# Optimization experiments

Measured on AMD Instinct MI355X. Metric: run time of the kernel, lower is better.

## Reference

```python
import jax, jax.numpy as jnp
import numpy as np

SIGMA_BOOST = 2.0   # sparse-hyper util.SIGMA_BOOST
EPSILON = 1e-6      # sparse-hyper util.EPSILON (10e-7)
B, N = 512, 16384   # batch, size


def setup_inputs() -> dict:
    key = jax.random.key(0)
    k1, k2, k3, k4, k5 = jax.random.split(key, 5)
    return {
        "x": jax.random.normal(k1, (B, N), jnp.float32),
        "noise": jax.random.normal(k2, (B, N, 2), jnp.float32),
        "pmeans": jax.random.normal(k3, (N, 2), jnp.float32),
        "psigmas": jax.random.normal(k4, (N,), jnp.float32),
        "pvalues": jax.random.normal(k5, (N,), jnp.float32),
    }


def reference(x, noise, pmeans, psigmas, pvalues):
    b, n = x.shape
    s = jnp.float32(n)  # square size (n, n); both dims equal
    # hyper(): transform_means = sigmoid * (size-1); transform_sigmas = (softplus(.+boost)+eps) * size
    means = jax.nn.sigmoid(pmeans)[None] * (s - 1.0)                    # (1, n, 2) -> bcast (b, n, 2)
    sigmas = (jax.nn.softplus(psigmas + SIGMA_BOOST) + EPSILON)[None, :, None] * s  # (1, n, 1)
    # Normal(means, sigmas).sample() -- non-differentiable sample
    samples = jax.lax.stop_gradient(means + sigmas * noise)             # (b, n, 2)
    # round, clamp to [0, n-1]
    indices = jnp.clip(jnp.round(samples).astype(jnp.int32), 0, n - 1)  # (b, n, 2)
    rows, cols = indices[..., 0], indices[..., 1]                       # (b, n) each
    values = jnp.broadcast_to(pvalues[None, :], (b, n))
    # sparse.contract: y[b, rows[b,t]] += values[b,t] * x[b, cols[b,t]]
    contrib = values * jnp.take_along_axis(x, cols, axis=1)             # (b, n)
    y = jnp.zeros((b, n), x.dtype).at[jnp.arange(b)[:, None], rows].add(contrib)
    return y
```

## Files before the change

kernel.cpp:

```cpp
#include <hip/hip_runtime.h>
#include <math.h>

#define SIGMA_BOOST 2.0f
#define EPSILON 1e-6f

__global__ void params_kernel(const float2* __restrict__ pmeans,
                              const float* __restrict__ psigmas,
                              const float* __restrict__ pvalues,
                              float4* __restrict__ params, int N) {
    int t = blockIdx.x * blockDim.x + threadIdx.x;
    if (t >= N) return;
    float2 pm = pmeans[t];
    float scale = (float)(N - 1);
    float m0 = __fmul_rn(__fdiv_rn(1.0f, __fadd_rn(1.0f, expf(-pm.x))), scale);
    float m1 = __fmul_rn(__fdiv_rn(1.0f, __fadd_rn(1.0f, expf(-pm.y))), scale);
    float z  = __fadd_rn(psigmas[t], SIGMA_BOOST);
    float sp = __fadd_rn(fmaxf(z, 0.0f), log1pf(expf(-fabsf(z))));
    float sg = __fmul_rn(__fadd_rn(sp, EPSILON), (float)N);
    params[t] = make_float4(m0, m1, sg, pvalues[t]);
}

template <bool INLINE_PARAMS>
__launch_bounds__(1024, 1)
__global__ void contract_kernel(const float* __restrict__ x,
                                const float2* __restrict__ noise,
                                const float4* __restrict__ params,
                                const float2* __restrict__ pmeans,
                                const float* __restrict__ psigmas,
                                const float* __restrict__ pvalues,
                                float* __restrict__ y, int N) {
    extern __shared__ float ly[];
    const int b = blockIdx.x;
    const int tid = threadIdx.x;
    const int nthr = blockDim.x;

    float4* ly4 = (float4*)ly;
    const int n4 = N >> 2;
    for (int i = tid; i < n4; i += nthr) ly4[i] = make_float4(0.f, 0.f, 0.f, 0.f);
    __syncthreads();

    const float*  xb = x + (size_t)b * N;
    const float2* nb = noise + (size_t)b * N;
    const float fN1 = (float)(N - 1);

    for (int t = tid; t < N; t += nthr) {
        float m0, m1, sg, pv;
        if (INLINE_PARAMS) {
            float2 pm = pmeans[t];
            float scale = (float)(N - 1);
            m0 = __fmul_rn(__fdiv_rn(1.0f, __fadd_rn(1.0f, expf(-pm.x))), scale);
            m1 = __fmul_rn(__fdiv_rn(1.0f, __fadd_rn(1.0f, expf(-pm.y))), scale);
            float z  = __fadd_rn(psigmas[t], SIGMA_BOOST);
            float sp = __fadd_rn(fmaxf(z, 0.0f), log1pf(expf(-fabsf(z))));
            sg = __fmul_rn(__fadd_rn(sp, EPSILON), (float)N);
            pv = pvalues[t];
        } else {
            float4 p = params[t];
            m0 = p.x; m1 = p.y; sg = p.z; pv = p.w;
        }
        float2 nz = nb[t];
        float s0 = __fadd_rn(m0, __fmul_rn(sg, nz.x));
        float s1 = __fadd_rn(m1, __fmul_rn(sg, nz.y));
        int row = (int)fminf(fmaxf(rintf(s0), 0.0f), fN1);
        int col = (int)fminf(fmaxf(rintf(s1), 0.0f), fN1);
        float contrib = __fmul_rn(pv, xb[col]);
        atomicAdd(&ly[row], contrib);
    }
    __syncthreads();

    float4* yb4 = (float4*)(y + (size_t)b * N);
    for (int i = tid; i < n4; i += nthr) yb4[i] = ly4[i];
}

extern "C" void kernel_launch(void* const* d_in, const int* in_sizes, int n_in,
                              void* d_out, int out_size, void* d_ws, size_t ws_size,
                              hipStream_t stream) {
    const float*  x       = (const float*)d_in[0];
    const float2* noise   = (const float2*)d_in[1];
    const float2* pmeans  = (const float2*)d_in[2];
    const float*  psigmas = (const float*)d_in[3];
    const float*  pvalues = (const float*)d_in[4];
    float* y = (float*)d_out;

    const int N = in_sizes[3];
    const int B = in_sizes[0] / N;

    const size_t params_bytes = (size_t)N * sizeof(float4);
    const bool use_ws = (ws_size >= params_bytes) && (d_ws != nullptr);

    const int block = 1024;
    const size_t lds_bytes = (size_t)N * sizeof(float);

    if (use_ws) {
        float4* params = (float4*)d_ws;
        params_kernel<<<(N + 255) / 256, 256, 0, stream>>>(pmeans, psigmas,
                                                           pvalues, params, N);
        contract_kernel<false><<<B, block, lds_bytes, stream>>>(
            x, noise, params, nullptr, nullptr, nullptr, y, N);
    } else {
        contract_kernel<true><<<B, block, lds_bytes, stream>>>(
            x, noise, nullptr, pmeans, psigmas, pvalues, y, N);
    }
}
```

Before: 163.4 us.

## Stage x row in LDS and unroll contract loop with vectorized noise loads

Copies each batch row of x into shared memory next to the accumulator, so the random column gathers hit LDS instead of global memory. The main loop is unrolled so each thread handles several consecutive elements, loading noise as float4 and grouping the gathers and atomics. Staging needs 128 KB of LDS per block and runs only when the device reports enough; otherwise a non-staged unroll-by-8 path runs. The extra LDS per block may lower occupancy, and each launch now makes host-side attribute queries.

```diff
diff --git a/kernel.cpp b/kernel.cpp
--- a/kernel.cpp
+++ b/kernel.cpp
@@ -4,12 +4,10 @@
 #define SIGMA_BOOST 2.0f
 #define EPSILON 1e-6f
 
-__global__ void params_kernel(const float2* __restrict__ pmeans,
-                              const float* __restrict__ psigmas,
-                              const float* __restrict__ pvalues,
-                              float4* __restrict__ params, int N) {
-    int t = blockIdx.x * blockDim.x + threadIdx.x;
-    if (t >= N) return;
+__device__ __forceinline__ float4 compute_param(const float2* __restrict__ pmeans,
+                                                const float* __restrict__ psigmas,
+                                                const float* __restrict__ pvalues,
+                                                int t, int N) {
     float2 pm = pmeans[t];
     float scale = (float)(N - 1);
     float m0 = __fmul_rn(__fdiv_rn(1.0f, __fadd_rn(1.0f, expf(-pm.x))), scale);
@@ -17,10 +15,18 @@
     float z  = __fadd_rn(psigmas[t], SIGMA_BOOST);
     float sp = __fadd_rn(fmaxf(z, 0.0f), log1pf(expf(-fabsf(z))));
     float sg = __fmul_rn(__fadd_rn(sp, EPSILON), (float)N);
-    params[t] = make_float4(m0, m1, sg, pvalues[t]);
+    return make_float4(m0, m1, sg, pvalues[t]);
 }
 
-template <bool INLINE_PARAMS>
+__global__ void params_kernel(const float2* __restrict__ pmeans,
+                              const float* __restrict__ psigmas,
+                              const float* __restrict__ pvalues,
+                              float4* __restrict__ params, int N) {
+    int t = blockIdx.x * blockDim.x + threadIdx.x;
+    if (t < N) params[t] = compute_param(pmeans, psigmas, pvalues, t, N);
+}
+
+template <bool STAGED, bool INLINE_PARAMS, int UNROLL>
 __launch_bounds__(1024, 1)
 __global__ void contract_kernel(const float* __restrict__ x,
                                 const float2* __restrict__ noise,
@@ -29,42 +35,62 @@
                                 const float* __restrict__ psigmas,
                                 const float* __restrict__ pvalues,
                                 float* __restrict__ y, int N) {
-    extern __shared__ float ly[];
+    extern __shared__ float lds[];
+    float* ly = lds;
+    float* lx = STAGED ? (lds + N) : nullptr;
+
     const int b = blockIdx.x;
     const int tid = threadIdx.x;
     const int nthr = blockDim.x;
+    const int n4 = N >> 2;
 
+    const float* xb = x + (size_t)b * N;
     float4* ly4 = (float4*)ly;
-    const int n4 = N >> 2;
-    for (int i = tid; i < n4; i += nthr) ly4[i] = make_float4(0.f, 0.f, 0.f, 0.f);
+    const float4* xb4 = (const float4*)xb;
+
+    if (STAGED) {
+        float4* lx4 = (float4*)lx;
+        for (int i = tid; i < n4; i += nthr) {
+            ly4[i] = make_float4(0.f, 0.f, 0.f, 0.f);
+            lx4[i] = xb4[i];
+        }
+    } else {
+        for (int i = tid; i < n4; i += nthr)
+            ly4[i] = make_float4(0.f, 0.f, 0.f, 0.f);
+    }
     __syncthreads();
 
-    const float*  xb = x + (size_t)b * N;
-    const float2* nb = noise + (size_t)b * N;
+    const float4* nb4 = (const float4*)(noise + (size_t)b * N);
     const float fN1 = (float)(N - 1);
 
-    for (int t = tid; t < N; t += nthr) {
-        float m0, m1, sg, pv;
-        if (INLINE_PARAMS) {
-            float2 pm = pmeans[t];
-            float scale = (float)(N - 1);
-            m0 = __fmul_rn(__fdiv_rn(1.0f, __fadd_rn(1.0f, expf(-pm.x))), scale);
-            m1 = __fmul_rn(__fdiv_rn(1.0f, __fadd_rn(1.0f, expf(-pm.y))), scale);
-            float z  = __fadd_rn(psigmas[t], SIGMA_BOOST);
-            float sp = __fadd_rn(fmaxf(z, 0.0f), log1pf(expf(-fabsf(z))));
-            sg = __fmul_rn(__fadd_rn(sp, EPSILON), (float)N);
-            pv = pvalues[t];
-        } else {
-            float4 p = params[t];
-            m0 = p.x; m1 = p.y; sg = p.z; pv = p.w;
+    for (int t0 = tid * UNROLL; t0 < N; t0 += nthr * UNROLL) {
+        float nz[2 * UNROLL];
+#pragma unroll
+        for (int u = 0; u < UNROLL / 2; ++u) {
+            float4 nv = nb4[(t0 >> 1) + u];
+            nz[4 * u + 0] = nv.x; nz[4 * u + 1] = nv.y;
+            nz[4 * u + 2] = nv.z; nz[4 * u + 3] = nv.w;
         }
-        float2 nz = nb[t];
-        float s0 = __fadd_rn(m0, __fmul_rn(sg, nz.x));
-        float s1 = __fadd_rn(m1, __fmul_rn(sg, nz.y));
-        int row = (int)fminf(fmaxf(rintf(s0), 0.0f), fN1);
-        int col = (int)fminf(fmaxf(rintf(s1), 0.0f), fN1);
-        float contrib = __fmul_rn(pv, xb[col]);
-        atomicAdd(&ly[row], contrib);
+        float4 p[UNROLL];
+#pragma unroll
+        for (int u = 0; u < UNROLL; ++u)
+            p[u] = INLINE_PARAMS ? compute_param(pmeans, psigmas, pvalues, t0 + u, N)
+                                 : params[t0 + u];
+        int r[UNROLL], c[UNROLL];
+#pragma unroll
+        for (int u = 0; u < UNROLL; ++u) {
+            float s0 = __fadd_rn(p[u].x, __fmul_rn(p[u].z, nz[2 * u + 0]));
+            float s1 = __fadd_rn(p[u].y, __fmul_rn(p[u].z, nz[2 * u + 1]));
+            r[u] = (int)fminf(fmaxf(rintf(s0), 0.0f), fN1);
+            c[u] = (int)fminf(fmaxf(rintf(s1), 0.0f), fN1);
+        }
+        float xv[UNROLL];
+#pragma unroll
+        for (int u = 0; u < UNROLL; ++u)
+            xv[u] = STAGED ? lx[c[u]] : xb[c[u]];
+#pragma unroll
+        for (int u = 0; u < UNROLL; ++u)
+            atomicAdd(&ly[r[u]], __fmul_rn(p[u].w, xv[u]));
     }
     __syncthreads();
 
@@ -89,16 +115,40 @@
     const bool use_ws = (ws_size >= params_bytes) && (d_ws != nullptr);
 
     const int block = 1024;
-    const size_t lds_bytes = (size_t)N * sizeof(float);
+    const size_t staged_lds = 2 * (size_t)N * sizeof(float);
+    const size_t acc_lds    = (size_t)N * sizeof(float);
 
-    if (use_ws) {
-        float4* params = (float4*)d_ws;
-        params_kernel<<<(N + 255) / 256, 256, 0, stream>>>(pmeans, psigmas,
-                                                           pvalues, params, N);
-        contract_kernel<false><<<B, block, lds_bytes, stream>>>(
-            x, noise, params, nullptr, nullptr, nullptr, y, N);
+    int dev = 0;
+    (void)hipGetDevice(&dev);
+    int max_lds = 0;
+    (void)hipDeviceGetAttribute(&max_lds, hipDeviceAttributeMaxSharedMemoryPerBlock, dev);
+    const bool staged = (size_t)max_lds >= staged_lds;
+
+    float4* params = (float4*)d_ws;
+    if (use_ws)
+        params_kernel<<<(N + 255) / 256, 256, 0, stream>>>(pmeans, psigmas, pvalues, params, N);
+
+    if (staged) {
+        if (use_ws) {
+            (void)hipFuncSetAttribute(
+                reinterpret_cast<const void*>(&contract_kernel<true, false, 4>),
+                hipFuncAttributeMaxDynamicSharedMemorySize, (int)staged_lds);
+            contract_kernel<true, false, 4><<<B, block, staged_lds, stream>>>(
+                x, noise, params, nullptr, nullptr, nullptr, y, N);
+        } else {
+            (void)hipFuncSetAttribute(
+                reinterpret_cast<const void*>(&contract_kernel<true, true, 4>),
+                hipFuncAttributeMaxDynamicSharedMemorySize, (int)staged_lds);
+            contract_kernel<true, true, 4><<<B, block, staged_lds, stream>>>(
+                x, noise, nullptr, pmeans, psigmas, pvalues, y, N);
+        }
     } else {
-        contract_kernel<true><<<B, block, lds_bytes, stream>>>(
-            x, noise, nullptr, pmeans, psigmas, pvalues, y, N);
+        if (use_ws) {
+            contract_kernel<false, false, 8><<<B, block, acc_lds, stream>>>(
+                x, noise, params, nullptr, nullptr, nullptr, y, N);
+        } else {
+            contract_kernel<false, true, 8><<<B, block, acc_lds, stream>>>(
+                x, noise, nullptr, pmeans, psigmas, pvalues, y, N);
+        }
     }
 }
```

Result: slower. 168.2 us (+3.0%).

## Split each row's output across two blocks and stage x as bf16 in LDS

Applied to the files above, without the earlier changes.

Adds a contract_split kernel that launches two blocks per batch row, each accumulating only half of the output rows in LDS. Every block converts the whole x row to bf16 and stages it in LDS, so the random column gathers read LDS instead of global memory. Noise is read as float4 with two loads in flight per iteration. The smaller LDS footprint allows more blocks per CU. The costs are that the full noise row is read twice per batch row, and the bf16 rounding of x reduces accuracy and may hurt tolerance.

```diff
diff --git a/kernel.cpp b/kernel.cpp
--- a/kernel.cpp
+++ b/kernel.cpp
@@ -4,12 +4,19 @@
 #define SIGMA_BOOST 2.0f
 #define EPSILON 1e-6f
 
-__global__ void params_kernel(const float2* __restrict__ pmeans,
-                              const float* __restrict__ psigmas,
-                              const float* __restrict__ pvalues,
-                              float4* __restrict__ params, int N) {
-    int t = blockIdx.x * blockDim.x + threadIdx.x;
-    if (t >= N) return;
+__device__ __forceinline__ unsigned short f32_to_bf16(float f) {
+    unsigned u = __float_as_uint(f);
+    unsigned rounding = 0x7FFFu + ((u >> 16) & 1u);
+    return (unsigned short)((u + rounding) >> 16);
+}
+__device__ __forceinline__ float bf16_to_f32(unsigned short h) {
+    return __uint_as_float((unsigned)h << 16);
+}
+
+__device__ __forceinline__ float4 compute_param(const float2* __restrict__ pmeans,
+                                                const float* __restrict__ psigmas,
+                                                const float* __restrict__ pvalues,
+                                                int t, int N) {
     float2 pm = pmeans[t];
     float scale = (float)(N - 1);
     float m0 = __fmul_rn(__fdiv_rn(1.0f, __fadd_rn(1.0f, expf(-pm.x))), scale);
@@ -17,7 +24,106 @@
     float z  = __fadd_rn(psigmas[t], SIGMA_BOOST);
     float sp = __fadd_rn(fmaxf(z, 0.0f), log1pf(expf(-fabsf(z))));
     float sg = __fmul_rn(__fadd_rn(sp, EPSILON), (float)N);
-    params[t] = make_float4(m0, m1, sg, pvalues[t]);
+    return make_float4(m0, m1, sg, pvalues[t]);
+}
+
+__global__ void params_kernel(const float2* __restrict__ pmeans,
+                              const float* __restrict__ psigmas,
+                              const float* __restrict__ pvalues,
+                              float4* __restrict__ params, int N) {
+    int t = blockIdx.x * blockDim.x + threadIdx.x;
+    if (t < N) params[t] = compute_param(pmeans, psigmas, pvalues, t, N);
+}
+
+template <bool INLINE_PARAMS>
+__launch_bounds__(1024, 8)
+__global__ void contract_split(const float* __restrict__ x,
+                               const float4* __restrict__ noise4,
+                               const float4* __restrict__ params,
+                               const float2* __restrict__ pmeans,
+                               const float* __restrict__ psigmas,
+                               const float* __restrict__ pvalues,
+                               float* __restrict__ y, int N, int B) {
+    const int nthr  = 1024;
+    const int tid   = threadIdx.x;
+    const int row   = (int)(blockIdx.x % (unsigned)B);
+    const int half  = (int)(blockIdx.x / (unsigned)B);
+    const int halfN = N >> 1;
+    const int rlo   = half * halfN;
+
+    extern __shared__ char lds[];
+    float* lacc = (float*)lds;
+    unsigned short* lx = (unsigned short*)(lds + (size_t)halfN * 4);
+
+    float4* lacc4 = (float4*)lacc;
+    const int h4 = halfN >> 2;
+    for (int i = tid; i < h4; i += nthr) lacc4[i] = make_float4(0.f, 0.f, 0.f, 0.f);
+
+    const float4* xb4 = (const float4*)(x + (size_t)row * N);
+    ushort4* lx4 = (ushort4*)lx;
+    const int n4 = N >> 2;
+    for (int i = tid; i < n4; i += nthr) {
+        float4 v = xb4[i];
+        ushort4 o;
+        o.x = f32_to_bf16(v.x);
+        o.y = f32_to_bf16(v.y);
+        o.z = f32_to_bf16(v.z);
+        o.w = f32_to_bf16(v.w);
+        lx4[i] = o;
+    }
+    __syncthreads();
+
+    const float4* nb4 = noise4 + (size_t)row * (size_t)(N >> 1);
+    const float fN1 = (float)(N - 1);
+    const int nf4 = N >> 11;
+
+    for (int u = 0; u < nf4; u += 2) {
+        const int j0 = tid + (u + 0) * nthr;
+        const int j1 = tid + (u + 1) * nthr;
+        float4 nv0 = nb4[j0];
+        float4 nv1 = nb4[j1];
+        float4 pa0, pb0, pa1, pb1;
+        if (INLINE_PARAMS) {
+            pa0 = compute_param(pmeans, psigmas, pvalues, 2 * j0,     N);
+            pb0 = compute_param(pmeans, psigmas, pvalues, 2 * j0 + 1, N);
+            pa1 = compute_param(pmeans, psigmas, pvalues, 2 * j1,     N);
+            pb1 = compute_param(pmeans, psigmas, pvalues, 2 * j1 + 1, N);
+        } else {
+            pa0 = params[2 * j0];
+            pb0 = params[2 * j0 + 1];
+            pa1 = params[2 * j1];
+            pb1 = params[2 * j1 + 1];
+        }
+
+        float sx[4], sy[4], pv[4];
+        sx[0] = __fadd_rn(pa0.x, __fmul_rn(pa0.z, nv0.x));
+        sy[0] = __fadd_rn(pa0.y, __fmul_rn(pa0.z, nv0.y));
+        pv[0] = pa0.w;
+        sx[1] = __fadd_rn(pb0.x, __fmul_rn(pb0.z, nv0.z));
+        sy[1] = __fadd_rn(pb0.y, __fmul_rn(pb0.z, nv0.w));
+        pv[1] = pb0.w;
+        sx[2] = __fadd_rn(pa1.x, __fmul_rn(pa1.z, nv1.x));
+        sy[2] = __fadd_rn(pa1.y, __fmul_rn(pa1.z, nv1.y));
+        pv[2] = pa1.w;
+        sx[3] = __fadd_rn(pb1.x, __fmul_rn(pb1.z, nv1.z));
+        sy[3] = __fadd_rn(pb1.y, __fmul_rn(pb1.z, nv1.w));
+        pv[3] = pb1.w;
+
+#pragma unroll
+        for (int k = 0; k < 4; ++k) {
+            int r = (int)fminf(fmaxf(rintf(sx[k]), 0.f), fN1);
+            int c = (int)fminf(fmaxf(rintf(sy[k]), 0.f), fN1);
+            unsigned rr = (unsigned)(r - rlo);
+            if (rr < (unsigned)halfN) {
+                float xv = bf16_to_f32(lx[c]);
+                atomicAdd(&lacc[rr], __fmul_rn(pv[k], xv));
+            }
+        }
+    }
+    __syncthreads();
+
+    float4* yb4 = (float4*)(y + (size_t)row * N + rlo);
+    for (int i = tid; i < h4; i += nthr) yb4[i] = lacc4[i];
 }
 
 template <bool INLINE_PARAMS>
@@ -44,27 +150,14 @@
     const float fN1 = (float)(N - 1);
 
     for (int t = tid; t < N; t += nthr) {
-        float m0, m1, sg, pv;
-        if (INLINE_PARAMS) {
-            float2 pm = pmeans[t];
-            float scale = (float)(N - 1);
-            m0 = __fmul_rn(__fdiv_rn(1.0f, __fadd_rn(1.0f, expf(-pm.x))), scale);
-            m1 = __fmul_rn(__fdiv_rn(1.0f, __fadd_rn(1.0f, expf(-pm.y))), scale);
-            float z  = __fadd_rn(psigmas[t], SIGMA_BOOST);
-            float sp = __fadd_rn(fmaxf(z, 0.0f), log1pf(expf(-fabsf(z))));
-            sg = __fmul_rn(__fadd_rn(sp, EPSILON), (float)N);
-            pv = pvalues[t];
-        } else {
-            float4 p = params[t];
-            m0 = p.x; m1 = p.y; sg = p.z; pv = p.w;
-        }
+        float4 p = INLINE_PARAMS ? compute_param(pmeans, psigmas, pvalues, t, N)
+                                 : params[t];
         float2 nz = nb[t];
-        float s0 = __fadd_rn(m0, __fmul_rn(sg, nz.x));
-        float s1 = __fadd_rn(m1, __fmul_rn(sg, nz.y));
-        int row = (int)fminf(fmaxf(rintf(s0), 0.0f), fN1);
-        int col = (int)fminf(fmaxf(rintf(s1), 0.0f), fN1);
-        float contrib = __fmul_rn(pv, xb[col]);
-        atomicAdd(&ly[row], contrib);
+        float s0 = __fadd_rn(p.x, __fmul_rn(p.z, nz.x));
+        float s1 = __fadd_rn(p.y, __fmul_rn(p.z, nz.y));
+        int r = (int)fminf(fmaxf(rintf(s0), 0.0f), fN1);
+        int c = (int)fminf(fmaxf(rintf(s1), 0.0f), fN1);
+        atomicAdd(&ly[r], __fmul_rn(p.w, xb[c]));
     }
     __syncthreads();
 
@@ -88,17 +181,27 @@
     const size_t params_bytes = (size_t)N * sizeof(float4);
     const bool use_ws = (ws_size >= params_bytes) && (d_ws != nullptr);
 
-    const int block = 1024;
-    const size_t lds_bytes = (size_t)N * sizeof(float);
-
-    if (use_ws) {
-        float4* params = (float4*)d_ws;
-        params_kernel<<<(N + 255) / 256, 256, 0, stream>>>(pmeans, psigmas,
-                                                           pvalues, params, N);
-        contract_kernel<false><<<B, block, lds_bytes, stream>>>(
-            x, noise, params, nullptr, nullptr, nullptr, y, N);
+    float4* params = (float4*)d_ws;
+    if (use_ws)
+        params_kernel<<<(N + 255) / 256, 256, 0, stream>>>(pmeans, psigmas, pvalues, params, N);
+
+    const size_t split_lds = 4 * (size_t)N;
+    if ((N % 4096) == 0 && split_lds <= 65536) {
+        if (use_ws) {
+            contract_split<false><<<2 * B, 1024, split_lds, stream>>>(
+                x, (const float4*)noise, params, nullptr, nullptr, nullptr, y, N, B);
+        } else {
+            contract_split<true><<<2 * B, 1024, split_lds, stream>>>(
+                x, (const float4*)noise, nullptr, pmeans, psigmas, pvalues, y, N, B);
+        }
     } else {
-        contract_kernel<true><<<B, block, lds_bytes, stream>>>(
-            x, noise, nullptr, pmeans, psigmas, pvalues, y, N);
-    }
-}
+        const size_t acc_lds = (size_t)N * sizeof(float);
+        if (use_ws) {
+            contract_kernel<false><<<B, 1024, acc_lds, stream>>>(
+                x, noise, params, nullptr, nullptr, nullptr, y, N);
+        } else {
+            contract_kernel<true><<<B, 1024, acc_lds, stream>>>(
+                x, noise, nullptr, pmeans, psigmas, pvalues, y, N);
+        }
+    }
+}
```

After: 179.9 us. 10.2% more time.
